# Kernel optimization log

Measured on AMD Instinct MI355X. Metric: run time of the kernel, lower is better.

The kernel has to match this reference:

```python
import jax, jax.numpy as jnp
import numpy as np

V, E, H, L = 32000, 512, 1024, 2
B, S = 16, 128


def _gru_cell(x, h, w_ih, w_hh, b_ih, b_hh):
    # PyTorch GRUCell: gates ordered (r, z, n), chunks of size H
    gi = x @ w_ih.T + b_ih            # (B, 3H)
    gh = h @ w_hh.T + b_hh            # (B, 3H)
    i_r, i_z, i_n = jnp.split(gi, 3, axis=-1)
    h_r, h_z, h_n = jnp.split(gh, 3, axis=-1)
    r = jax.nn.sigmoid(i_r + h_r)
    z = jax.nn.sigmoid(i_z + h_z)
    n = jnp.tanh(i_n + r * h_n)
    return (1.0 - z) * n + z * h


def setup_inputs() -> dict:
    key = jax.random.key(0)
    ks = jax.random.split(key, 16)
    s = lambda fan: 1.0 / np.sqrt(fan)
    inp = {
        "hidden": jax.random.normal(ks[0], (L, B, H), jnp.float32),
        "trg": jax.random.randint(ks[1], (B, S), 0, V),
        "embedding": jax.random.normal(ks[2], (V, E), jnp.float32) * 0.02,
        # layer 0 GRU (input_size=E)
        "w_ih0": jax.random.uniform(ks[3], (3 * H, E), jnp.float32, -s(H), s(H)),
        "w_hh0": jax.random.uniform(ks[4], (3 * H, H), jnp.float32, -s(H), s(H)),
        "b_ih0": jnp.zeros((3 * H,), jnp.float32),
        "b_hh0": jnp.zeros((3 * H,), jnp.float32),
        # layer 1 GRU (input_size=H)
        "w_ih1": jax.random.uniform(ks[5], (3 * H, H), jnp.float32, -s(H), s(H)),
        "w_hh1": jax.random.uniform(ks[6], (3 * H, H), jnp.float32, -s(H), s(H)),
        "b_ih1": jnp.zeros((3 * H,), jnp.float32),
        "b_hh1": jnp.zeros((3 * H,), jnp.float32),
        # output projection MLP: Linear(H,H) -> ReLU -> Linear(H,E)
        "w1": jax.random.uniform(ks[7], (H, H), jnp.float32, -s(H), s(H)),
        "b1": jnp.zeros((H,), jnp.float32),
        "w2": jax.random.uniform(ks[8], (E, H), jnp.float32, -s(H), s(H)),
        "b2": jnp.zeros((E,), jnp.float32),
        # generator bias (weight tied to embedding)
        "b_gen": jnp.zeros((V,), jnp.float32),
    }
    return inp


def reference(hidden, trg, embedding, w_ih0, w_hh0, b_ih0, b_hh0,
              w_ih1, w_hh1, b_ih1, b_hh1, w1, b1, w2, b2, b_gen):
    def step(h, tok):
        # h: (L, B, H); tok: (B,)
        x = embedding[tok]                                 # (B, E)
        h0 = _gru_cell(x, h[0], w_ih0, w_hh0, b_ih0, b_hh0)
        h1 = _gru_cell(h0, h[1], w_ih1, w_hh1, b_ih1, b_hh1)
        new_h = jnp.stack([h0, h1], axis=0)
        out = jax.nn.relu(h1 @ w1.T + b1) @ w2.T + b2      # (B, E)
        logit = out @ embedding.T + b_gen                  # (B, V) weight-tied
        return new_h, logit

    _, logits = jax.lax.scan(step, hidden, trg.T)          # (S, B, V)
    return jnp.transpose(logits, (1, 0, 2))                # (B, S, V)
```

## Files before the change

kernel.cpp:

```cpp
#include <hip/hip_runtime.h>
#include <math.h>

#define Sn 128
#define Bn 16
#define Hn 1024
#define En 512
#define Vn 32000
#define H3 3072

typedef _Float16 h16;
typedef __attribute__((ext_vector_type(2))) _Float16 h16x2;
typedef __attribute__((ext_vector_type(4))) _Float16 h16x4;
typedef __attribute__((ext_vector_type(8))) _Float16 h16x8;
typedef __attribute__((ext_vector_type(4))) float f32x4;

#if defined(__has_builtin)
#if __has_builtin(__builtin_amdgcn_fdot2)
#define HAS_FDOT2 1
#endif
#endif

__device__ __forceinline__ float dot8(h16x8 a, h16x8 b, float acc) {
#ifdef HAS_FDOT2
  h16x2 a0 = {a[0], a[1]}, b0 = {b[0], b[1]};
  acc = __builtin_amdgcn_fdot2(a0, b0, acc, false);
  h16x2 a1 = {a[2], a[3]}, b1 = {b[2], b[3]};
  acc = __builtin_amdgcn_fdot2(a1, b1, acc, false);
  h16x2 a2 = {a[4], a[5]}, b2 = {b[4], b[5]};
  acc = __builtin_amdgcn_fdot2(a2, b2, acc, false);
  h16x2 a3 = {a[6], a[7]}, b3 = {b[6], b[7]};
  acc = __builtin_amdgcn_fdot2(a3, b3, acc, false);
#else
#pragma unroll
  for (int i = 0; i < 8; ++i) acc = fmaf((float)a[i], (float)b[i], acc);
#endif
  return acc;
}

#define Q_EMB   4096000
#define Q_WIH0  (Q_EMB + 393216)
#define Q_W1    (Q_WIH0 + 262144)
#define Q_W2    (Q_W1 + 131072)
#define Q_WHH0  (Q_W2 + 786432)
#define Q_WIH1  (Q_WHH0 + 786432)
#define Q_WHH1  (Q_WIH1 + 786432)
#define Q_HID   (Q_WHH1 + 8192)
__global__ __launch_bounds__(256) void cvt_all_k(
    const float* __restrict__ emb, const float* __restrict__ wih0,
    const float* __restrict__ w1, const float* __restrict__ w2,
    const float* __restrict__ whh0, const float* __restrict__ wih1,
    const float* __restrict__ whh1, const float* __restrict__ hid,
    h16* __restrict__ E, h16* __restrict__ A, h16* __restrict__ B1,
    h16* __restrict__ B2, h16* __restrict__ D0, h16* __restrict__ D1,
    h16* __restrict__ D2, h16* __restrict__ HD)
{
  int i = blockIdx.x * 256 + threadIdx.x;
  const float* s; h16* d; int o;
  if      (i < Q_EMB)  { s = emb;  d = E;  o = i; }
  else if (i < Q_WIH0) { s = wih0; d = A;  o = i - Q_EMB; }
  else if (i < Q_W1)   { s = w1;   d = B1; o = i - Q_WIH0; }
  else if (i < Q_W2)   { s = w2;   d = B2; o = i - Q_W1; }
  else if (i < Q_WHH0) { s = whh0; d = D0; o = i - Q_W2; }
  else if (i < Q_WIH1) { s = wih1; d = D1; o = i - Q_WHH0; }
  else if (i < Q_WHH1) { s = whh1; d = D2; o = i - Q_WIH1; }
  else                 { s = hid;  d = HD; o = i - Q_WHH1; }
  float4 v = *(const float4*)(s + (size_t)o * 4);
  h16x4 ov = { (h16)v.x, (h16)v.y, (h16)v.z, (h16)v.w };
  *(h16x4*)(d + (size_t)o * 4) = ov;
}

__global__ void embed_k(const int* __restrict__ trg, const float* __restrict__ emb,
                        h16* __restrict__ Xh) {
  int t = blockIdx.x;
  int s = t >> 4, b = t & 15;
  int tok = trg[b * Sn + s];
  const float* src = emb + (size_t)tok * En;
  int e = threadIdx.x * 4;
  float4 v = *(const float4*)(src + e);
  h16x4 o = { (h16)v.x, (h16)v.y, (h16)v.z, (h16)v.w };
  *(h16x4*)(Xh + (size_t)t * En + e) = o;
}

template<int OUT_MODE, bool RELU, bool SWZ>
__global__ __launch_bounds__(256) void gemm_bt(
    const h16* __restrict__ A, const h16* __restrict__ B,
    const float* __restrict__ bias, void* __restrict__ C,
    int M, int N, int K)
{
  __shared__ h16 As[128 * 64];
  __shared__ h16 Bs[128 * 64];
  int tid = threadIdx.x;
  int l = tid & 63, wv = tid >> 6;
  int wr = wv >> 1, wc = wv & 1;

  int work = blockIdx.x;
  if (SWZ) { int q = gridDim.x >> 3; work = (work & 7) * q + (work >> 3); }
  int nMp = M >> 7;
  int brow = (work % nMp) << 7;
  int bcol = (work / nMp) << 7;

  f32x4 acc[4][4];
#pragma unroll
  for (int m = 0; m < 4; ++m)
#pragma unroll
    for (int n = 0; n < 4; ++n) acc[m][n] = (f32x4){0.f, 0.f, 0.f, 0.f};

  int nkt = K >> 6;
  for (int kt = 0; kt < nkt; ++kt) {
    const h16* Ag = A + (size_t)brow * K + kt * 64;
    const h16* Bg = B + (size_t)bcol * K + kt * 64;
#pragma unroll
    for (int c = tid; c < 2048; c += 256) {
      int half = c >> 10;
      int cc = c & 1023;
      int row = cc >> 3, slot = cc & 7;
      const h16* src = (half ? Bg : Ag) + (size_t)row * K + slot * 8;
      uint4 v = *(const uint4*)src;
      h16* dst = (half ? Bs : As) + row * 64 + ((slot ^ (row & 7)) << 3);
      *(uint4*)dst = v;
    }
    __syncthreads();
#pragma unroll
    for (int kk = 0; kk < 2; ++kk) {
      h16x8 af[4], bfr[4];
      int rb = wr * 64 + (l & 15);
      int cb2 = wc * 64 + (l & 15);
      int slot = kk * 4 + (l >> 4);
#pragma unroll
      for (int m = 0; m < 4; ++m) {
        int r = rb + m * 16;
        af[m] = *(const h16x8*)&As[r * 64 + ((slot ^ (r & 7)) << 3)];
      }
#pragma unroll
      for (int n = 0; n < 4; ++n) {
        int r = cb2 + n * 16;
        bfr[n] = *(const h16x8*)&Bs[r * 64 + ((slot ^ (r & 7)) << 3)];
      }
#pragma unroll
      for (int m = 0; m < 4; ++m)
#pragma unroll
        for (int n = 0; n < 4; ++n)
          acc[m][n] = __builtin_amdgcn_mfma_f32_16x16x32_f16(af[m], bfr[n], acc[m][n], 0, 0, 0);
    }
    __syncthreads();
  }

#pragma unroll
  for (int m = 0; m < 4; ++m) {
    int row0 = brow + wr * 64 + m * 16 + ((l >> 4) << 2);
#pragma unroll
    for (int n = 0; n < 4; ++n) {
      int col = bcol + wc * 64 + n * 16 + (l & 15);
      float bv = bias ? bias[col] : 0.f;
#pragma unroll
      for (int i = 0; i < 4; ++i) {
        int row = row0 + i;
        float v = acc[m][n][i] + bv;
        if (RELU) v = fmaxf(v, 0.f);
        if (OUT_MODE == 1) {
          ((h16*)C)[(size_t)row * N + col] = (h16)v;
        } else if (OUT_MODE == 2) {
          int rr = ((row & 15) << 7) + (row >> 4);
          ((float*)C)[(size_t)rr * N + col] = v;
        } else {
          ((float*)C)[(size_t)row * N + col] = v;
        }
      }
    }
  }
}

__global__ __launch_bounds__(256, 1) void gemm_bt256(
    const h16* __restrict__ A, const h16* __restrict__ B,
    const float* __restrict__ bias, float* __restrict__ C,
    int M, int N, int K)
{
  __shared__ h16 As[128 * 64];
  __shared__ h16 Bs[256 * 64];
  int tid = threadIdx.x;
  int l = tid & 63, wv = tid >> 6;
  int wr = wv >> 1, wc = wv & 1;

  int work = blockIdx.x;
  int q = gridDim.x >> 3; work = (work & 7) * q + (work >> 3);
  int nMp = M >> 7;
  int brow = (work % nMp) << 7;
  int bcol = (work / nMp) << 8;

  f32x4 acc[4][8];
#pragma unroll
  for (int m = 0; m < 4; ++m)
#pragma unroll
    for (int n = 0; n < 8; ++n) acc[m][n] = (f32x4){0.f, 0.f, 0.f, 0.f};

  int nkt = K >> 6;
  for (int kt = 0; kt < nkt; ++kt) {
    const h16* Ag = A + (size_t)brow * K + kt * 64;
    const h16* Bg = B + (size_t)bcol * K + kt * 64;
#pragma unroll
    for (int c = tid; c < 3072; c += 256) {
      int isB = (c >= 1024);
      int cc = isB ? (c - 1024) : c;
      int row = cc >> 3, slot = cc & 7;
      const h16* src = (isB ? Bg : Ag) + (size_t)row * K + slot * 8;
      uint4 v = *(const uint4*)src;
      h16* dst = (isB ? Bs : As) + row * 64 + ((slot ^ (row & 7)) << 3);
      *(uint4*)dst = v;
    }
    __syncthreads();
#pragma unroll
    for (int kk = 0; kk < 2; ++kk) {
      h16x8 af[4], bfr[8];
      int rb = wr * 64 + (l & 15);
      int cb2 = wc * 128 + (l & 15);
      int slot = kk * 4 + (l >> 4);
#pragma unroll
      for (int m = 0; m < 4; ++m) {
        int r = rb + m * 16;
        af[m] = *(const h16x8*)&As[r * 64 + ((slot ^ (r & 7)) << 3)];
      }
#pragma unroll
      for (int n = 0; n < 8; ++n) {
        int r = cb2 + n * 16;
        bfr[n] = *(const h16x8*)&Bs[r * 64 + ((slot ^ (r & 7)) << 3)];
      }
#pragma unroll
      for (int m = 0; m < 4; ++m)
#pragma unroll
        for (int n = 0; n < 8; ++n)
          acc[m][n] = __builtin_amdgcn_mfma_f32_16x16x32_f16(af[m], bfr[n], acc[m][n], 0, 0, 0);
    }
    __syncthreads();
  }

#pragma unroll
  for (int m = 0; m < 4; ++m) {
    int row0 = brow + wr * 64 + m * 16 + ((l >> 4) << 2);
#pragma unroll
    for (int n = 0; n < 8; ++n) {
      int col = bcol + wc * 128 + n * 16 + (l & 15);
      float bv = bias[col];
#pragma unroll
      for (int i = 0; i < 4; ++i) {
        int row = row0 + i;
        int rr = ((row & 15) << 7) + (row >> 4);
        C[(size_t)rr * N + col] = acc[m][n][i] + bv;
      }
    }
  }
}

__device__ __forceinline__ void gbar2(int* __restrict__ flags, int target, int bid) {
  __syncthreads();
  int tid = threadIdx.x;
  if (tid == 0)
    __hip_atomic_store(&flags[bid << 5], target, __ATOMIC_RELAXED, __HIP_MEMORY_SCOPE_AGENT);
  if (tid < 64) {
    int q = tid << 2;
    for (;;) {
      int m0 = __hip_atomic_load(&flags[(q + 0) << 5], __ATOMIC_RELAXED, __HIP_MEMORY_SCOPE_AGENT);
      int m1 = __hip_atomic_load(&flags[(q + 1) << 5], __ATOMIC_RELAXED, __HIP_MEMORY_SCOPE_AGENT);
      int m2 = __hip_atomic_load(&flags[(q + 2) << 5], __ATOMIC_RELAXED, __HIP_MEMORY_SCOPE_AGENT);
      int m3 = __hip_atomic_load(&flags[(q + 3) << 5], __ATOMIC_RELAXED, __HIP_MEMORY_SCOPE_AGENT);
      if (m0 >= target && m1 >= target && m2 >= target && m3 >= target) break;
      __builtin_amdgcn_s_sleep(1);
    }
    asm volatile("" ::: "memory");
  }
  __syncthreads();
}

__global__ __launch_bounds__(768, 1) void gru_persist3(
    const float* __restrict__ gi0,
    const float* __restrict__ hidden,
    const h16* __restrict__ hinit16,
    const h16* __restrict__ whh0, const float* __restrict__ bhh0,
    const h16* __restrict__ wih1, const float* __restrict__ bih1,
    const h16* __restrict__ whh1, const float* __restrict__ bhh1,
    h16* __restrict__ h0ring,
    h16* __restrict__ H1A,
    int* __restrict__ flags)
{
  extern __shared__ h16 ldsw[];
  __shared__ float cmb[4][3][16];

  int bid = blockIdx.x;
  int tid = threadIdx.x;
  int base = bid << 2;

  __threadfence();

  for (int i = tid; i < 4608; i += 768) {
    int r = i >> 7, ch = i & 127;
    int c = r / 9, g = r % 9;
    const h16* src = (g < 3) ? whh0 + (((size_t)(g * 1024 + base + c)) << 10)
                   : (g < 6) ? wih1 + (((size_t)((g - 3) * 1024 + base + c)) << 10)
                             : whh1 + (((size_t)((g - 6) * 1024 + base + c)) << 10);
    *(uint4*)(ldsw + r * 1024 + ch * 8) = *(const uint4*)(src + ch * 8);
  }

  int wv = tid >> 6;
  int l = tid & 63;
  int c = wv / 3, role = wv % 3;
  int j = base + c;
  int b = l >> 2, p = l & 3;
  const h16* wR = ldsw + (c * 9 + role * 3) * 1024;

  float bA = 0, bB = 0, bC = 0, bD = 0, bE = 0, bF = 0;
  if (role == 0) { bA = bhh0[j]; bB = bhh0[1024 + j]; bC = bhh0[2048 + j]; }
  if (role == 2) { bA = bih1[j]; bB = bih1[1024 + j]; bC = bih1[2048 + j];
                   bD = bhh1[j]; bE = bhh1[1024 + j]; bF = bhh1[2048 + j]; }
  float hprev = (role == 0) ? hidden[(b << 10) + j]
              : (role == 2) ? hidden[16384 + (b << 10) + j] : 0.f;
  __syncthreads();

  for (int s = 0; s <= Sn; ++s) {
    bool active = (role == 0) ? (s < Sn) : (s >= 1);
    float giR = 0.f, giZ = 0.f, giN = 0.f;
    if (role == 0 && p == 0 && s < Sn) {
      const float* gi = gi0 + (size_t)((s << 4) + b) * H3;
      giR = gi[j]; giZ = gi[1024 + j]; giN = gi[2048 + j];
    }
    float a0 = 0.f, a1 = 0.f, a2 = 0.f;
    if (active) {
      const h16* hrow = (role <= 1)
          ? ((s == 0) ? hinit16 : h0ring + (((size_t)(s - 1)) << 14))
          : ((s <= 1) ? hinit16 + 16384 : H1A + (((size_t)(s - 2)) << 14));
      const h16* hb = hrow + (b << 10);
#pragma unroll 8
      for (int t = 0; t < 32; ++t) {
        int k = (p << 3) + (t << 5);
        h16x8 h8 = *(const h16x8*)(hb + k);
        a0 = dot8(h8, *(const h16x8*)(wR + k), a0);
        a1 = dot8(h8, *(const h16x8*)(wR + 1024 + k), a1);
        a2 = dot8(h8, *(const h16x8*)(wR + 2048 + k), a2);
      }
      a0 += __shfl_xor(a0, 1, 64); a0 += __shfl_xor(a0, 2, 64);
      a1 += __shfl_xor(a1, 1, 64); a1 += __shfl_xor(a1, 2, 64);
      a2 += __shfl_xor(a2, 1, 64); a2 += __shfl_xor(a2, 2, 64);
      if (role == 1 && p == 0) { cmb[c][0][b] = a0; cmb[c][1][b] = a1; cmb[c][2][b] = a2; }
    }
    __syncthreads();
    if (active && p == 0) {
      if (role == 0) {
        float r = 1.f / (1.f + expf(-(giR + a0 + bA)));
        float z = 1.f / (1.f + expf(-(giZ + a1 + bB)));
        float n = tanhf(giN + r * (a2 + bC));
        float out = (1.f - z) * n + z * hprev;
        hprev = out;
        h16 hv = (h16)out; unsigned short us; __builtin_memcpy(&us, &hv, 2);
        __hip_atomic_store((unsigned short*)h0ring + (((size_t)s) << 14) + (b << 10) + j,
                           us, __ATOMIC_RELAXED, __HIP_MEMORY_SCOPE_AGENT);
      } else if (role == 2) {
        float air = cmb[c][0][b], aiz = cmb[c][1][b], ain = cmb[c][2][b];
        float r = 1.f / (1.f + expf(-(air + bA + a0 + bD)));
        float z = 1.f / (1.f + expf(-(aiz + bB + a1 + bE)));
        float n = tanhf(ain + bC + r * (a2 + bF));
        float out = (1.f - z) * n + z * hprev;
        hprev = out;
        h16 hv = (h16)out; unsigned short us; __builtin_memcpy(&us, &hv, 2);
        __hip_atomic_store((unsigned short*)H1A + (((size_t)(s - 1)) << 14) + (b << 10) + j,
                           us, __ATOMIC_RELAXED, __HIP_MEMORY_SCOPE_AGENT);
      }
    }
    if (s < Sn) gbar2(flags, s + 1, bid);
  }
}

extern "C" void kernel_launch(void* const* d_in, const int* in_sizes, int n_in,
                              void* d_out, int out_size, void* d_ws, size_t ws_size,
                              hipStream_t stream) {
  const float* hidden = (const float*)d_in[0];
  const int*   trg    = (const int*)d_in[1];
  const float* emb    = (const float*)d_in[2];
  const float* w_ih0  = (const float*)d_in[3];
  const float* w_hh0  = (const float*)d_in[4];
  const float* b_ih0  = (const float*)d_in[5];
  const float* b_hh0  = (const float*)d_in[6];
  const float* w_ih1  = (const float*)d_in[7];
  const float* w_hh1  = (const float*)d_in[8];
  const float* b_ih1  = (const float*)d_in[9];
  const float* b_hh1  = (const float*)d_in[10];
  const float* w1     = (const float*)d_in[11];
  const float* b1     = (const float*)d_in[12];
  const float* w2     = (const float*)d_in[13];
  const float* b2     = (const float*)d_in[14];
  const float* b_gen  = (const float*)d_in[15];

  char* ws = (char*)d_ws;
  size_t off = 0;
  float* GI0    = (float*)(ws + off); off += (size_t)Sn * Bn * H3 * 4;
  h16* Xh       = (h16*)(ws + off);   off += (size_t)Sn * Bn * En * 2;
  h16* embH     = (h16*)(ws + off);   off += (size_t)Vn * En * 2;
  h16* wih0H    = (h16*)(ws + off);   off += (size_t)H3 * En * 2;
  h16* w1H      = (h16*)(ws + off);   off += (size_t)Hn * Hn * 2;
  h16* w2H      = (h16*)(ws + off);   off += (size_t)En * Hn * 2;
  h16* whh0H    = (h16*)(ws + off);   off += (size_t)H3 * Hn * 2;
  h16* wih1H    = (h16*)(ws + off);   off += (size_t)H3 * Hn * 2;
  h16* whh1H    = (h16*)(ws + off);   off += (size_t)H3 * Hn * 2;
  h16* H1A      = (h16*)(ws + off);   off += (size_t)Sn * Bn * Hn * 2;
  h16* h0ring   = (h16*)(ws + off);   off += (size_t)Sn * Bn * Hn * 2;
  h16* hinit16  = (h16*)(ws + off);   off += (size_t)2 * Bn * Hn * 2;
  int* flags    = (int*)(ws + off);   off += 32768;
  h16* Tb = (h16*)GI0;
  h16* Ub = (h16*)((char*)GI0 + (8u << 20));

  cvt_all_k<<<28320, 256, 0, stream>>>(emb, w_ih0, w1, w2, w_hh0, w_ih1, w_hh1, hidden,
                                       embH, wih0H, w1H, w2H, whh0H, wih1H, whh1H, hinit16);
  embed_k<<<Sn * Bn, 128, 0, stream>>>(trg, emb, Xh);

  gemm_bt<0, false, true><<<384, 256, 0, stream>>>(Xh, wih0H, b_ih0, GI0, Sn * Bn, H3, En);

  (void)hipMemsetAsync(flags, 0, 32768, stream);
  const int LDSZ = 36 * 1024 * 2;
  (void)hipFuncSetAttribute(reinterpret_cast<const void*>(gru_persist3),
                            hipFuncAttributeMaxDynamicSharedMemorySize, LDSZ);
  gru_persist3<<<256, 768, LDSZ, stream>>>(GI0, hidden, hinit16,
                                           whh0H, b_hh0, wih1H, b_ih1, whh1H, b_hh1,
                                           h0ring, H1A, flags);

  gemm_bt<1, true,  true><<<128,  256, 0, stream>>>(H1A, w1H, b1, Tb, Sn * Bn, Hn, Hn);
  gemm_bt<1, false, true><<<64,   256, 0, stream>>>(Tb, w2H, b2, Ub, Sn * Bn, En, Hn);
  gemm_bt256<<<2000, 256, 0, stream>>>(Ub, embH, b_gen, (float*)d_out, Sn * Bn, Vn, En);
}
```

Baseline: 1.484 ms.

## Rewrite persistent GRU recurrence with MFMA, register-resident weights, split layer pipelines

Replaces the 256-block persistent GRU kernel, which computed dot products with fdot2 from LDS-resident weights, with a 96-block kernel that keeps recurrent weights in registers and uses 16x16x32 f16 MFMA instructions. Layer 0 and layer 1 run on separate block groups. Each group waits only on point-to-point flags for the data it consumes instead of a global barrier across all blocks, so layer 1 can trail layer 0 in a pipeline. The costs are heavy register pressure (32 h16x8 fragments per lane), fewer active CUs, and busy-wait polling with no sleep.

```diff
diff --git a/kernel.cpp b/kernel.cpp
--- a/kernel.cpp
+++ b/kernel.cpp
@@ -7,35 +7,13 @@
 #define En 512
 #define Vn 32000
 #define H3 3072
+#define NL0 32
+#define NL1 64
 
 typedef _Float16 h16;
-typedef __attribute__((ext_vector_type(2))) _Float16 h16x2;
 typedef __attribute__((ext_vector_type(4))) _Float16 h16x4;
 typedef __attribute__((ext_vector_type(8))) _Float16 h16x8;
 typedef __attribute__((ext_vector_type(4))) float f32x4;
-
-#if defined(__has_builtin)
-#if __has_builtin(__builtin_amdgcn_fdot2)
-#define HAS_FDOT2 1
-#endif
-#endif
-
-__device__ __forceinline__ float dot8(h16x8 a, h16x8 b, float acc) {
-#ifdef HAS_FDOT2
-  h16x2 a0 = {a[0], a[1]}, b0 = {b[0], b[1]};
-  acc = __builtin_amdgcn_fdot2(a0, b0, acc, false);
-  h16x2 a1 = {a[2], a[3]}, b1 = {b[2], b[3]};
-  acc = __builtin_amdgcn_fdot2(a1, b1, acc, false);
-  h16x2 a2 = {a[4], a[5]}, b2 = {b[4], b[5]};
-  acc = __builtin_amdgcn_fdot2(a2, b2, acc, false);
-  h16x2 a3 = {a[6], a[7]}, b3 = {b[6], b[7]};
-  acc = __builtin_amdgcn_fdot2(a3, b3, acc, false);
-#else
-#pragma unroll
-  for (int i = 0; i < 8; ++i) acc = fmaf((float)a[i], (float)b[i], acc);
-#endif
-  return acc;
-}
 
 #define Q_EMB   4096000
 #define Q_WIH0  (Q_EMB + 393216)
@@ -250,27 +228,7 @@
   }
 }
 
-__device__ __forceinline__ void gbar2(int* __restrict__ flags, int target, int bid) {
-  __syncthreads();
-  int tid = threadIdx.x;
-  if (tid == 0)
-    __hip_atomic_store(&flags[bid << 5], target, __ATOMIC_RELAXED, __HIP_MEMORY_SCOPE_AGENT);
-  if (tid < 64) {
-    int q = tid << 2;
-    for (;;) {
-      int m0 = __hip_atomic_load(&flags[(q + 0) << 5], __ATOMIC_RELAXED, __HIP_MEMORY_SCOPE_AGENT);
-      int m1 = __hip_atomic_load(&flags[(q + 1) << 5], __ATOMIC_RELAXED, __HIP_MEMORY_SCOPE_AGENT);
-      int m2 = __hip_atomic_load(&flags[(q + 2) << 5], __ATOMIC_RELAXED, __HIP_MEMORY_SCOPE_AGENT);
-      int m3 = __hip_atomic_load(&flags[(q + 3) << 5], __ATOMIC_RELAXED, __HIP_MEMORY_SCOPE_AGENT);
-      if (m0 >= target && m1 >= target && m2 >= target && m3 >= target) break;
-      __builtin_amdgcn_s_sleep(1);
-    }
-    asm volatile("" ::: "memory");
-  }
-  __syncthreads();
-}
-
-__global__ __launch_bounds__(768, 1) void gru_persist3(
+__global__ __launch_bounds__(384, 1) void gru_mfma(
     const float* __restrict__ gi0,
     const float* __restrict__ hidden,
     const h16* __restrict__ hinit16,
@@ -281,89 +239,142 @@
     h16* __restrict__ H1A,
     int* __restrict__ flags)
 {
-  extern __shared__ h16 ldsw[];
-  __shared__ float cmb[4][3][16];
-
+  __shared__ float exch[5][256];
   int bid = blockIdx.x;
   int tid = threadIdx.x;
-  int base = bid << 2;
+  int w = tid >> 6, l = tid & 63;
+  int li = l & 15;
+  int ko = (l >> 4) << 3;
+  int b0 = (l >> 4) << 2;
 
   __threadfence();
 
-  for (int i = tid; i < 4608; i += 768) {
-    int r = i >> 7, ch = i & 127;
-    int c = r / 9, g = r % 9;
-    const h16* src = (g < 3) ? whh0 + (((size_t)(g * 1024 + base + c)) << 10)
-                   : (g < 6) ? wih1 + (((size_t)((g - 3) * 1024 + base + c)) << 10)
-                             : whh1 + (((size_t)((g - 6) * 1024 + base + c)) << 10);
-    *(uint4*)(ldsw + r * 1024 + ch * 8) = *(const uint4*)(src + ch * 8);
-  }
-
-  int wv = tid >> 6;
-  int l = tid & 63;
-  int c = wv / 3, role = wv % 3;
-  int j = base + c;
-  int b = l >> 2, p = l & 3;
-  const h16* wR = ldsw + (c * 9 + role * 3) * 1024;
-
-  float bA = 0, bB = 0, bC = 0, bD = 0, bE = 0, bF = 0;
-  if (role == 0) { bA = bhh0[j]; bB = bhh0[1024 + j]; bC = bhh0[2048 + j]; }
-  if (role == 2) { bA = bih1[j]; bB = bih1[1024 + j]; bC = bih1[2048 + j];
-                   bD = bhh1[j]; bE = bhh1[1024 + j]; bF = bhh1[2048 + j]; }
-  float hprev = (role == 0) ? hidden[(b << 10) + j]
-              : (role == 2) ? hidden[16384 + (b << 10) + j] : 0.f;
-  __syncthreads();
-
-  for (int s = 0; s <= Sn; ++s) {
-    bool active = (role == 0) ? (s < Sn) : (s >= 1);
-    float giR = 0.f, giZ = 0.f, giN = 0.f;
-    if (role == 0 && p == 0 && s < Sn) {
-      const float* gi = gi0 + (size_t)((s << 4) + b) * H3;
-      giR = gi[j]; giZ = gi[1024 + j]; giN = gi[2048 + j];
-    }
-    float a0 = 0.f, a1 = 0.f, a2 = 0.f;
-    if (active) {
-      const h16* hrow = (role <= 1)
-          ? ((s == 0) ? hinit16 : h0ring + (((size_t)(s - 1)) << 14))
-          : ((s <= 1) ? hinit16 + 16384 : H1A + (((size_t)(s - 2)) << 14));
-      const h16* hb = hrow + (b << 10);
-#pragma unroll 8
-      for (int t = 0; t < 32; ++t) {
-        int k = (p << 3) + (t << 5);
-        h16x8 h8 = *(const h16x8*)(hb + k);
-        a0 = dot8(h8, *(const h16x8*)(wR + k), a0);
-        a1 = dot8(h8, *(const h16x8*)(wR + 1024 + k), a1);
-        a2 = dot8(h8, *(const h16x8*)(wR + 2048 + k), a2);
-      }
-      a0 += __shfl_xor(a0, 1, 64); a0 += __shfl_xor(a0, 2, 64);
-      a1 += __shfl_xor(a1, 1, 64); a1 += __shfl_xor(a1, 2, 64);
-      a2 += __shfl_xor(a2, 1, 64); a2 += __shfl_xor(a2, 2, 64);
-      if (role == 1 && p == 0) { cmb[c][0][b] = a0; cmb[c][1][b] = a1; cmb[c][2][b] = a2; }
-    }
-    __syncthreads();
-    if (active && p == 0) {
-      if (role == 0) {
-        float r = 1.f / (1.f + expf(-(giR + a0 + bA)));
-        float z = 1.f / (1.f + expf(-(giZ + a1 + bB)));
-        float n = tanhf(giN + r * (a2 + bC));
-        float out = (1.f - z) * n + z * hprev;
-        hprev = out;
-        h16 hv = (h16)out; unsigned short us; __builtin_memcpy(&us, &hv, 2);
-        __hip_atomic_store((unsigned short*)h0ring + (((size_t)s) << 14) + (b << 10) + j,
-                           us, __ATOMIC_RELAXED, __HIP_MEMORY_SCOPE_AGENT);
-      } else if (role == 2) {
-        float air = cmb[c][0][b], aiz = cmb[c][1][b], ain = cmb[c][2][b];
-        float r = 1.f / (1.f + expf(-(air + bA + a0 + bD)));
-        float z = 1.f / (1.f + expf(-(aiz + bB + a1 + bE)));
-        float n = tanhf(ain + bC + r * (a2 + bF));
-        float out = (1.f - z) * n + z * hprev;
-        hprev = out;
-        h16 hv = (h16)out; unsigned short us; __builtin_memcpy(&us, &hv, 2);
-        __hip_atomic_store((unsigned short*)H1A + (((size_t)(s - 1)) << 14) + (b << 10) + j,
-                           us, __ATOMIC_RELAXED, __HIP_MEMORY_SCOPE_AGENT);
-      }
-    }
-    if (s < Sn) gbar2(flags, s + 1, bid);
+  int* fL0 = flags;
+  int* fL1 = flags + 1024;
+
+  if (bid < NL0) {
+    int gate = w >> 1, ch = w & 1;
+    int j = bid * 32 + ch * 16 + li;
+    h16x8 Bf[32];
+    {
+      const h16* wp = whh0 + ((size_t)((gate << 10) + j) << 10) + ko;
+#pragma unroll
+      for (int t = 0; t < 32; ++t) Bf[t] = *(const h16x8*)(wp + t * 32);
+    }
+    float bR = 0.f, bZ = 0.f, bN = 0.f;
+    float hprev[4];
+    if (gate == 2) {
+      bR = bhh0[j]; bZ = bhh0[1024 + j]; bN = bhh0[2048 + j];
+#pragma unroll
+      for (int i = 0; i < 4; ++i) hprev[i] = hidden[((b0 + i) << 10) + j];
+    }
+
+    for (int s = 0; s < Sn; ++s) {
+      if (s > 0) {
+        if (w == 0 && l < NL0)
+          while (__hip_atomic_load(&fL0[l << 5], __ATOMIC_RELAXED, __HIP_MEMORY_SCOPE_AGENT) < s) {}
+        __syncthreads();
+        asm volatile("" ::: "memory");
+      }
+      float gr[4], gz[4], gn[4];
+      if (gate == 2) {
+        const float* gb = gi0 + ((size_t)s << 4) * H3;
+#pragma unroll
+        for (int i = 0; i < 4; ++i) {
+          const float* g = gb + (size_t)(b0 + i) * H3 + j;
+          gr[i] = g[0]; gz[i] = g[1024]; gn[i] = g[2048];
+        }
+      }
+      const h16* hsrc = (s == 0) ? hinit16 : h0ring + (((size_t)(s - 1)) << 14);
+      const h16* Ap = hsrc + (li << 10) + ko;
+      f32x4 acc = (f32x4){0.f, 0.f, 0.f, 0.f};
+#pragma unroll
+      for (int t = 0; t < 32; ++t)
+        acc = __builtin_amdgcn_mfma_f32_16x16x32_f16(*(const h16x8*)(Ap + t * 32), Bf[t], acc, 0, 0, 0);
+      if (w < 4) {
+#pragma unroll
+        for (int i = 0; i < 4; ++i) exch[w][((b0 + i) << 4) + li] = acc[i];
+      }
+      __syncthreads();
+      if (gate == 2) {
+#pragma unroll
+        for (int i = 0; i < 4; ++i) {
+          int e = ((b0 + i) << 4) + li;
+          float r = 1.f / (1.f + expf(-(exch[ch][e] + bR + gr[i])));
+          float z = 1.f / (1.f + expf(-(exch[2 + ch][e] + bZ + gz[i])));
+          float n = tanhf(gn[i] + r * (acc[i] + bN));
+          float out = (1.f - z) * n + z * hprev[i];
+          hprev[i] = out;
+          h16 hv = (h16)out; unsigned short us; __builtin_memcpy(&us, &hv, 2);
+          __hip_atomic_store((unsigned short*)h0ring + (((size_t)s) << 14) + ((b0 + i) << 10) + j,
+                             us, __ATOMIC_RELAXED, __HIP_MEMORY_SCOPE_AGENT);
+        }
+      }
+      __syncthreads();
+      if (tid == 0)
+        __hip_atomic_store(&fL0[bid << 5], s + 1, __ATOMIC_RELAXED, __HIP_MEMORY_SCOPE_AGENT);
+    }
+  } else {
+    int bl = bid - NL0;
+    int j = (bl << 4) + li;
+    int isHH = (w >= 3);
+    int gate = isHH ? (w - 3) : w;
+    h16x8 Bf[32];
+    {
+      const h16* wsrc = isHH ? whh1 : wih1;
+      const h16* wp = wsrc + ((size_t)((gate << 10) + j) << 10) + ko;
+#pragma unroll
+      for (int t = 0; t < 32; ++t) Bf[t] = *(const h16x8*)(wp + t * 32);
+    }
+    float bIR = 0.f, bIZ = 0.f, bIN = 0.f, bHR = 0.f, bHZ = 0.f, bHN = 0.f;
+    float hprev[4];
+    if (w == 5) {
+      bIR = bih1[j]; bIZ = bih1[1024 + j]; bIN = bih1[2048 + j];
+      bHR = bhh1[j]; bHZ = bhh1[1024 + j]; bHN = bhh1[2048 + j];
+#pragma unroll
+      for (int i = 0; i < 4; ++i) hprev[i] = hidden[16384 + ((b0 + i) << 10) + j];
+    }
+
+    for (int s = 1; s <= Sn; ++s) {
+      if (w == 0) {
+        if (l < NL0)
+          while (__hip_atomic_load(&fL0[l << 5], __ATOMIC_RELAXED, __HIP_MEMORY_SCOPE_AGENT) < s) {}
+      } else if (w == 1 && s >= 2) {
+        while (__hip_atomic_load(&fL1[l << 5], __ATOMIC_RELAXED, __HIP_MEMORY_SCOPE_AGENT) < s) {}
+      }
+      __syncthreads();
+      asm volatile("" ::: "memory");
+      const h16* hsrc = isHH
+          ? ((s == 1) ? hinit16 + 16384 : H1A + (((size_t)(s - 2)) << 14))
+          : (h0ring + (((size_t)(s - 1)) << 14));
+      const h16* Ap = hsrc + (li << 10) + ko;
+      f32x4 acc = (f32x4){0.f, 0.f, 0.f, 0.f};
+#pragma unroll
+      for (int t = 0; t < 32; ++t)
+        acc = __builtin_amdgcn_mfma_f32_16x16x32_f16(*(const h16x8*)(Ap + t * 32), Bf[t], acc, 0, 0, 0);
+      if (w < 5) {
+#pragma unroll
+        for (int i = 0; i < 4; ++i) exch[w][((b0 + i) << 4) + li] = acc[i];
+      }
+      __syncthreads();
+      if (w == 5) {
+#pragma unroll
+        for (int i = 0; i < 4; ++i) {
+          int e = ((b0 + i) << 4) + li;
+          float r = 1.f / (1.f + expf(-(exch[0][e] + bIR + exch[3][e] + bHR)));
+          float z = 1.f / (1.f + expf(-(exch[1][e] + bIZ + exch[4][e] + bHZ)));
+          float n = tanhf(exch[2][e] + bIN + r * (acc[i] + bHN));
+          float out = (1.f - z) * n + z * hprev[i];
+          hprev[i] = out;
+          h16 hv = (h16)out; unsigned short us; __builtin_memcpy(&us, &hv, 2);
+          __hip_atomic_store((unsigned short*)H1A + (((size_t)(s - 1)) << 14) + ((b0 + i) << 10) + j,
+                             us, __ATOMIC_RELAXED, __HIP_MEMORY_SCOPE_AGENT);
+        }
+      }
+      __syncthreads();
+      if (tid == 0)
+        __hip_atomic_store(&fL1[bl << 5], s + 1, __ATOMIC_RELAXED, __HIP_MEMORY_SCOPE_AGENT);
+    }
   }
 }
 
@@ -401,7 +412,7 @@
   h16* H1A      = (h16*)(ws + off);   off += (size_t)Sn * Bn * Hn * 2;
   h16* h0ring   = (h16*)(ws + off);   off += (size_t)Sn * Bn * Hn * 2;
   h16* hinit16  = (h16*)(ws + off);   off += (size_t)2 * Bn * Hn * 2;
-  int* flags    = (int*)(ws + off);   off += 32768;
+  int* flags    = (int*)(ws + off);   off += 16384;
   h16* Tb = (h16*)GI0;
   h16* Ub = (h16*)((char*)GI0 + (8u << 20));
 
@@ -411,13 +422,10 @@
 
   gemm_bt<0, false, true><<<384, 256, 0, stream>>>(Xh, wih0H, b_ih0, GI0, Sn * Bn, H3, En);
 
-  (void)hipMemsetAsync(flags, 0, 32768, stream);
-  const int LDSZ = 36 * 1024 * 2;
-  (void)hipFuncSetAttribute(reinterpret_cast<const void*>(gru_persist3),
-                            hipFuncAttributeMaxDynamicSharedMemorySize, LDSZ);
-  gru_persist3<<<256, 768, LDSZ, stream>>>(GI0, hidden, hinit16,
-                                           whh0H, b_hh0, wih1H, b_ih1, whh1H, b_hh1,
-                                           h0ring, H1A, flags);
+  (void)hipMemsetAsync(flags, 0, 16384, stream);
+  gru_mfma<<<NL0 + NL1, 384, 0, stream>>>(GI0, hidden, hinit16,
+                                          whh0H, b_hh0, wih1H, b_ih1, whh1H, b_hh1,
+                                          h0ring, H1A, flags);
 
   gemm_bt<1, true,  true><<<128,  256, 0, stream>>>(H1A, w1H, b1, Tb, Sn * Bn, Hn, Hn);
   gemm_bt<1, false, true><<<64,   256, 0, stream>>>(Tb, w2H, b2, Ub, Sn * Bn, En, Hn);
```

Result: no change. 1.488 ms (+0.3%).
